# Optimization experiments

Hardware: AMD Instinct MI355X
Metric: run time of the kernel (lower is better)

## Reference

```python
import jax, jax.numpy as jnp
import numpy as np

N_NODES = 100000
N_EDGES = 1000000
NUM_GRAPHS = 500
EPS = 1e-5


def gcn_conv(x, src, dst, W, b, n_nodes):
    # PyG GCNConv: h = x @ W, symmetric norm with self-loops, aggregate at dst, add bias
    h = x @ W
    deg = jnp.zeros((n_nodes,), h.dtype).at[dst].add(1.0) + 1.0  # in-degree + self-loop
    dis = jax.lax.rsqrt(deg)
    msg = h[src] * (dis[src] * dis[dst])[:, None]               # [E, F] gather
    agg = jnp.zeros_like(h).at[dst].add(msg)                    # scatter-add
    return agg + h * (dis * dis)[:, None] + b                   # self-loop term + bias


def bn_eval(x, g, be, m, v):
    return (x - m) * jax.lax.rsqrt(v + EPS) * g + be


def setup_inputs() -> dict:
    key = jax.random.key(0)
    ks = jax.random.split(key, 8)
    edge_index = jax.random.randint(ks[0], (2, N_EDGES), 0, N_NODES, dtype=jnp.int32)
    batch = jnp.sort(jax.random.randint(ks[1], (N_NODES,), 0, NUM_GRAPHS, dtype=jnp.int32))
    d_in, h1, h2, hc, nc = 64, 64, 32, 16, 2
    return {
        "x": jax.random.normal(ks[2], (N_NODES, d_in), jnp.float32),
        "edge_index": edge_index,
        "batch": batch,
        "W1": jax.random.normal(ks[3], (d_in, h1), jnp.float32) / np.sqrt(d_in),
        "b1": jnp.zeros((h1,), jnp.float32),
        "g1": jnp.ones((h1,), jnp.float32),
        "be1": jnp.zeros((h1,), jnp.float32),
        "m1": jnp.zeros((h1,), jnp.float32),
        "v1": jnp.ones((h1,), jnp.float32),
        "W2": jax.random.normal(ks[4], (h1, h2), jnp.float32) / np.sqrt(h1),
        "b2": jnp.zeros((h2,), jnp.float32),
        "g2": jnp.ones((h2,), jnp.float32),
        "be2": jnp.zeros((h2,), jnp.float32),
        "m2": jnp.zeros((h2,), jnp.float32),
        "v2": jnp.ones((h2,), jnp.float32),
        "Wc1": jax.random.normal(ks[5], (h2, hc), jnp.float32) / np.sqrt(h2),
        "bc1": jnp.zeros((hc,), jnp.float32),
        "Wc2": jax.random.normal(ks[6], (hc, nc), jnp.float32) / np.sqrt(hc),
        "bc2": jnp.zeros((nc,), jnp.float32),
    }


def reference(x, edge_index, batch, W1, b1, g1, be1, m1, v1,
              W2, b2, g2, be2, m2, v2, Wc1, bc1, Wc2, bc2):
    src, dst = edge_index[0], edge_index[1]
    n = x.shape[0]
    # encoder layer 1: GCNConv -> BN(eval) -> ReLU  (dropout off in eval)
    h = jax.nn.relu(bn_eval(gcn_conv(x, src, dst, W1, b1, n), g1, be1, m1, v1))
    # encoder layer 2
    h = jax.nn.relu(bn_eval(gcn_conv(h, src, dst, W2, b2, n), g2, be2, m2, v2))
    # global mean pool over graphs
    sums = jax.ops.segment_sum(h, batch, num_segments=NUM_GRAPHS)
    cnts = jax.ops.segment_sum(jnp.ones((n,), h.dtype), batch, num_segments=NUM_GRAPHS)
    z = sums / jnp.maximum(cnts, 1.0)[:, None]                  # [NUM_GRAPHS, h2]
    # classifier MLP
    return jax.nn.relu(z @ Wc1 + bc1) @ Wc2 + bc2               # [NUM_GRAPHS, num_classes]
```

## Files before the change

kernel.cpp:

```cpp
#include <hip/hip_runtime.h>
#include <hip/hip_bf16.h>


#define CHUNK 4096
#define CAP   4096

typedef float floatx2 __attribute__((ext_vector_type(2)));

__global__ __launch_bounds__(256) void k_binpairs2(
    const int* __restrict__ src, const int* __restrict__ dst,
    int* __restrict__ bucketCursor, unsigned* __restrict__ pairs, int E) {
    __shared__ int lh[512];
    __shared__ int lbase[512];
    for (int i = threadIdx.x; i < 512; i += 256) lh[i] = 0;
    __syncthreads();
    int base = blockIdx.x * CHUNK;
    for (int i = threadIdx.x; i < CHUNK; i += 256) {
        int e = base + i;
        if (e < E) atomicAdd(&lh[dst[e] >> 8], 1);
    }
    __syncthreads();
    for (int i = threadIdx.x; i < 512; i += 256) {
        int c = lh[i];
        lbase[i] = c ? atomicAdd(&bucketCursor[i], c) : 0;
        lh[i] = 0;
    }
    __syncthreads();
    for (int i = threadIdx.x; i < CHUNK; i += 256) {
        int e = base + i;
        if (e < E) {
            int d = dst[e];
            int b = d >> 8;
            int r = atomicAdd(&lh[b], 1);
            pairs[(size_t)b * CAP + lbase[b] + r] =
                ((unsigned)src[e] << 8) | (unsigned)(d & 255);
        }
    }
}

__global__ __launch_bounds__(256) void k_csr2(
    const unsigned* __restrict__ pairs, const int* __restrict__ bucketCursor,
    int* __restrict__ rowStart, int* __restrict__ rowEnd,
    float* __restrict__ dis, int* __restrict__ perm, int n,
    float* __restrict__ sums, int nSums) {
    __shared__ int cnt[256];
    __shared__ int s[256];
    __shared__ int cur[256];
    int b = blockIdx.x, tid = threadIdx.x;
    int zi = b * 256 + tid;
    if (zi < nSums) sums[zi] = 0.f;
    int total = bucketCursor[b];
    size_t base = (size_t)b * CAP;
    cnt[tid] = 0;
    __syncthreads();
    for (int i = tid; i < total; i += 256) atomicAdd(&cnt[pairs[base + i] & 255], 1);
    __syncthreads();
    int v = cnt[tid];
    s[tid] = v;
    __syncthreads();
    for (int off = 1; off < 256; off <<= 1) {
        int t = (tid >= off) ? s[tid - off] : 0;
        __syncthreads();
        s[tid] += t;
        __syncthreads();
    }
    int excl = s[tid] - v;
    int node = b * 256 + tid;
    if (node < n) {
        rowStart[node] = (int)base + excl;
        rowEnd[node]   = (int)base + excl + v;
        dis[node] = rsqrtf((float)v + 1.0f);
    }
    cur[tid] = excl;
    __syncthreads();
    for (int i = tid; i < total; i += 256) {
        unsigned pr = pairs[base + i];
        int lo = pr & 255;
        int slot = atomicAdd(&cur[lo], 1);
        perm[base + slot] = (int)(pr >> 8);
    }
}

__global__ __launch_bounds__(256) void k_gemm64(
    const float* __restrict__ x, const float* __restrict__ W,
    const float* __restrict__ dis, unsigned char* __restrict__ hs8, int n) {
    __shared__ float Ws[64 * 64];
    __shared__ float xs[128][65];
    const int tid = threadIdx.x;
    for (int i = tid * 4; i < 4096; i += 1024)
        *(float4*)&Ws[i] = *(const float4*)&W[i];
    const int base = blockIdx.x * 128;
    for (int i = tid; i < 2048; i += 256) {
        int r = i >> 4;
        int k = (i & 15) * 4;
        int row = base + r;
        float4 xv = (row < n) ? *(const float4*)&x[(size_t)row * 64 + k]
                              : make_float4(0.f, 0.f, 0.f, 0.f);
        xs[r][k] = xv.x; xs[r][k + 1] = xv.y; xs[r][k + 2] = xv.z; xs[r][k + 3] = xv.w;
    }
    __syncthreads();
    const int cg = tid & 7;
    const int rg = tid >> 3;
    float acc[4][8] = {};
#pragma unroll 4
    for (int k = 0; k < 64; ++k) {
        float w8[8];
        *(float4*)&w8[0] = *(const float4*)&Ws[k * 64 + cg * 8];
        *(float4*)&w8[4] = *(const float4*)&Ws[k * 64 + cg * 8 + 4];
        float x4[4];
#pragma unroll
        for (int rr = 0; rr < 4; ++rr) x4[rr] = xs[rg * 4 + rr][k];
#pragma unroll
        for (int rr = 0; rr < 4; ++rr)
#pragma unroll
            for (int cc = 0; cc < 8; ++cc)
                acc[rr][cc] = fmaf(x4[rr], w8[cc], acc[rr][cc]);
    }
#pragma unroll
    for (int rr = 0; rr < 4; ++rr) {
        int row = base + rg * 4 + rr;
        if (row >= n) break;
        float d = dis[row];
        int q0 = __builtin_amdgcn_cvt_pk_fp8_f32(acc[rr][0] * d, acc[rr][1] * d, 0, false);
        q0 = __builtin_amdgcn_cvt_pk_fp8_f32(acc[rr][2] * d, acc[rr][3] * d, q0, true);
        int q1 = __builtin_amdgcn_cvt_pk_fp8_f32(acc[rr][4] * d, acc[rr][5] * d, 0, false);
        q1 = __builtin_amdgcn_cvt_pk_fp8_f32(acc[rr][6] * d, acc[rr][7] * d, q1, true);
        uint2 q = {(unsigned)q0, (unsigned)q1};
        *(uint2*)&hs8[(size_t)row * 64 + cg * 8] = q;
    }
}

__device__ __forceinline__ void unpack8(uint2 u, float* a) {
    floatx2 p0 = __builtin_amdgcn_cvt_pk_f32_fp8(u.x, false);
    floatx2 p1 = __builtin_amdgcn_cvt_pk_f32_fp8(u.x, true);
    floatx2 p2 = __builtin_amdgcn_cvt_pk_f32_fp8(u.y, false);
    floatx2 p3 = __builtin_amdgcn_cvt_pk_f32_fp8(u.y, true);
    a[0] = p0[0]; a[1] = p0[1]; a[2] = p1[0]; a[3] = p1[1];
    a[4] = p2[0]; a[5] = p2[1]; a[6] = p3[0]; a[7] = p3[1];
}

__global__ __launch_bounds__(256) void k_g64f8_gemm32(
    const unsigned char* __restrict__ hs8, const int* __restrict__ rowStart,
    const int* __restrict__ rowEnd, const int* __restrict__ perm,
    const float* __restrict__ dis,
    const float* __restrict__ b, const float* __restrict__ g,
    const float* __restrict__ be, const float* __restrict__ m,
    const float* __restrict__ v, const float* __restrict__ W2,
    unsigned char* __restrict__ hs2f8, int n) {
    __shared__ float W2s[64 * 32];
    __shared__ float actS[32][68];
    for (int i = threadIdx.x * 4; i < 2048; i += 1024)
        *(float4*)&W2s[i] = *(const float4*)&W2[i];
    __syncthreads();

    const uint2* hsu = (const uint2*)hs8;
    int c = threadIdx.x & 7;
    int ln = threadIdx.x >> 3;
    int node = (blockIdx.x * 256 + threadIdx.x) >> 3;
    if (node >= n) return;
    int r0 = rowStart[node], r1 = rowEnd[node];
    float d = dis[node];
    float a[8];
    unpack8(hsu[(size_t)node * 8 + c], a);
    int e = r0;
    for (; e + 7 < r1; e += 8) {
        int s0 = perm[e],     s1 = perm[e + 1], s2 = perm[e + 2], s3 = perm[e + 3];
        int s4 = perm[e + 4], s5 = perm[e + 5], s6 = perm[e + 6], s7 = perm[e + 7];
        uint2 u0 = hsu[(size_t)s0 * 8 + c];
        uint2 u1 = hsu[(size_t)s1 * 8 + c];
        uint2 u2 = hsu[(size_t)s2 * 8 + c];
        uint2 u3 = hsu[(size_t)s3 * 8 + c];
        uint2 u4 = hsu[(size_t)s4 * 8 + c];
        uint2 u5 = hsu[(size_t)s5 * 8 + c];
        uint2 u6 = hsu[(size_t)s6 * 8 + c];
        uint2 u7 = hsu[(size_t)s7 * 8 + c];
        float t[8];
#pragma unroll
        for (int j = 0; j < 8; ++j) {
            uint2 u = j == 0 ? u0 : j == 1 ? u1 : j == 2 ? u2 : j == 3 ? u3
                    : j == 4 ? u4 : j == 5 ? u5 : j == 6 ? u6 : u7;
            unpack8(u, t);
#pragma unroll
            for (int q = 0; q < 8; ++q) a[q] += t[q];
        }
    }
    for (; e < r1; ++e) {
        float t[8];
        unpack8(hsu[(size_t)perm[e] * 8 + c], t);
#pragma unroll
        for (int q = 0; q < 8; ++q) a[q] += t[q];
    }
    int f = 8 * c;
    float y[8];
#pragma unroll
    for (int h = 0; h < 2; ++h) {
        float4 gv = *(const float4*)&g[f + 4 * h];
        float4 vv = *(const float4*)&v[f + 4 * h];
        float4 bv = *(const float4*)&b[f + 4 * h];
        float4 mv = *(const float4*)&m[f + 4 * h];
        float4 bev = *(const float4*)&be[f + 4 * h];
        float sc0 = gv.x * rsqrtf(vv.x + 1e-5f), sc1 = gv.y * rsqrtf(vv.y + 1e-5f);
        float sc2 = gv.z * rsqrtf(vv.z + 1e-5f), sc3 = gv.w * rsqrtf(vv.w + 1e-5f);
        float y0 = fmaf(a[4 * h + 0] * d, sc0, (bv.x - mv.x) * sc0 + bev.x);
        float y1 = fmaf(a[4 * h + 1] * d, sc1, (bv.y - mv.y) * sc1 + bev.y);
        float y2 = fmaf(a[4 * h + 2] * d, sc2, (bv.z - mv.z) * sc2 + bev.z);
        float y3 = fmaf(a[4 * h + 3] * d, sc3, (bv.w - mv.w) * sc3 + bev.w);
        y[4 * h + 0] = y0 > 0.f ? y0 : 0.f;
        y[4 * h + 1] = y1 > 0.f ? y1 : 0.f;
        y[4 * h + 2] = y2 > 0.f ? y2 : 0.f;
        y[4 * h + 3] = y3 > 0.f ? y3 : 0.f;
    }
    *(float4*)&actS[ln][f]     = *(float4*)&y[0];
    *(float4*)&actS[ln][f + 4] = *(float4*)&y[4];

    float o0 = 0.f, o1 = 0.f, o2 = 0.f, o3 = 0.f;
#pragma unroll
    for (int k = 0; k < 64; ++k) {
        float av = actS[ln][k];
        float4 w = *(const float4*)&W2s[k * 32 + 4 * c];
        o0 = fmaf(av, w.x, o0);
        o1 = fmaf(av, w.y, o1);
        o2 = fmaf(av, w.z, o2);
        o3 = fmaf(av, w.w, o3);
    }
    int q = __builtin_amdgcn_cvt_pk_fp8_f32(o0 * d, o1 * d, 0, false);
    q = __builtin_amdgcn_cvt_pk_fp8_f32(o2 * d, o3 * d, q, true);
    *(unsigned*)&hs2f8[(size_t)node * 32 + 4 * c] = (unsigned)q;
}

__global__ __launch_bounds__(256) void k_g32f8_pool(
    const unsigned char* __restrict__ hs8, const int* __restrict__ rowStart,
    const int* __restrict__ rowEnd, const int* __restrict__ perm,
    const float* __restrict__ dis,
    const float* __restrict__ b, const float* __restrict__ g,
    const float* __restrict__ be, const float* __restrict__ m,
    const float* __restrict__ v, const int* __restrict__ batch,
    float* __restrict__ sums, float* __restrict__ cntG, int n) {
    __shared__ float lsum[64][32];
    __shared__ float lcnt[64];
    const uint2* hsu = (const uint2*)hs8;
    int tid = threadIdx.x;
    int c = tid & 3;
    int node = (blockIdx.x * 256 + tid) >> 2;
    int base = blockIdx.x * 64;
    bool valid = node < n;

    int lastNode = min(base + 63, n - 1);
    int g0 = batch[base < n ? base : n - 1];
    int span = batch[lastNode] - g0 + 1;
    bool ldsPath = span <= 64;

    if (ldsPath) {
        for (int i = tid; i < span * 32; i += 256) lsum[i >> 5][i & 31] = 0.f;
        for (int i = tid; i < span; i += 256) lcnt[i] = 0.f;
    }
    __syncthreads();

    float y[8];
    int f = 8 * c;
    if (valid) {
        int r0 = rowStart[node], r1 = rowEnd[node];
        float d = dis[node];
        float a[8];
        unpack8(hsu[(size_t)node * 4 + c], a);
        int e = r0;
        for (; e + 7 < r1; e += 8) {
            int s0 = perm[e],     s1 = perm[e + 1], s2 = perm[e + 2], s3 = perm[e + 3];
            int s4 = perm[e + 4], s5 = perm[e + 5], s6 = perm[e + 6], s7 = perm[e + 7];
            uint2 u0 = hsu[(size_t)s0 * 4 + c];
            uint2 u1 = hsu[(size_t)s1 * 4 + c];
            uint2 u2 = hsu[(size_t)s2 * 4 + c];
            uint2 u3 = hsu[(size_t)s3 * 4 + c];
            uint2 u4 = hsu[(size_t)s4 * 4 + c];
            uint2 u5 = hsu[(size_t)s5 * 4 + c];
            uint2 u6 = hsu[(size_t)s6 * 4 + c];
            uint2 u7 = hsu[(size_t)s7 * 4 + c];
            float t[8];
#pragma unroll
            for (int j = 0; j < 8; ++j) {
                uint2 u = j == 0 ? u0 : j == 1 ? u1 : j == 2 ? u2 : j == 3 ? u3
                        : j == 4 ? u4 : j == 5 ? u5 : j == 6 ? u6 : u7;
                unpack8(u, t);
#pragma unroll
                for (int q = 0; q < 8; ++q) a[q] += t[q];
            }
        }
        for (; e < r1; ++e) {
            float t[8];
            unpack8(hsu[(size_t)perm[e] * 4 + c], t);
#pragma unroll
            for (int q = 0; q < 8; ++q) a[q] += t[q];
        }
#pragma unroll
        for (int h = 0; h < 2; ++h) {
            float4 gv = *(const float4*)&g[f + 4 * h];
            float4 vv = *(const float4*)&v[f + 4 * h];
            float4 bv = *(const float4*)&b[f + 4 * h];
            float4 mv = *(const float4*)&m[f + 4 * h];
            float4 bev = *(const float4*)&be[f + 4 * h];
            float sc0 = gv.x * rsqrtf(vv.x + 1e-5f), sc1 = gv.y * rsqrtf(vv.y + 1e-5f);
            float sc2 = gv.z * rsqrtf(vv.z + 1e-5f), sc3 = gv.w * rsqrtf(vv.w + 1e-5f);
            float y0 = fmaf(a[4 * h + 0] * d, sc0, (bv.x - mv.x) * sc0 + bev.x);
            float y1 = fmaf(a[4 * h + 1] * d, sc1, (bv.y - mv.y) * sc1 + bev.y);
            float y2 = fmaf(a[4 * h + 2] * d, sc2, (bv.z - mv.z) * sc2 + bev.z);
            float y3 = fmaf(a[4 * h + 3] * d, sc3, (bv.w - mv.w) * sc3 + bev.w);
            y[4 * h + 0] = y0 > 0.f ? y0 : 0.f;
            y[4 * h + 1] = y1 > 0.f ? y1 : 0.f;
            y[4 * h + 2] = y2 > 0.f ? y2 : 0.f;
            y[4 * h + 3] = y3 > 0.f ? y3 : 0.f;
        }
        int bg = batch[node];
        if (ldsPath) {
            int gl = bg - g0;
#pragma unroll
            for (int j = 0; j < 8; ++j) atomicAdd(&lsum[gl][f + j], y[j]);
            if (c == 0) atomicAdd(&lcnt[gl], 1.f);
        } else {
#pragma unroll
            for (int j = 0; j < 8; ++j) atomicAdd(&sums[(size_t)bg * 32 + f + j], y[j]);
            if (c == 0) atomicAdd(&cntG[bg], 1.f);
        }
    }
    __syncthreads();
    if (ldsPath) {
        for (int i = tid; i < span * 32; i += 256) {
            int gs = i >> 5, ff = i & 31;
            float vl = lsum[gs][ff];
            if (vl != 0.f) atomicAdd(&sums[(size_t)(g0 + gs) * 32 + ff], vl);
        }
        for (int i = tid; i < span; i += 256) {
            float vl = lcnt[i];
            if (vl != 0.f) atomicAdd(&cntG[g0 + i], vl);
        }
    }
}

__global__ void k_mlp(const float* __restrict__ sums, const float* __restrict__ cnt,
                      const float* __restrict__ Wc1, const float* __restrict__ bc1,
                      const float* __restrict__ Wc2, const float* __restrict__ bc2,
                      float* __restrict__ out, int G) {
    int g = blockIdx.x * blockDim.x + threadIdx.x;
    if (g >= G) return;
    float c = cnt[g];
    c = c < 1.f ? 1.f : c;
    float inv = 1.f / c;
    float z[32];
#pragma unroll
    for (int j = 0; j < 32; ++j) z[j] = sums[(size_t)g * 32 + j] * inv;
    float o0 = bc2[0], o1 = bc2[1];
#pragma unroll
    for (int k = 0; k < 16; ++k) {
        float t = bc1[k];
#pragma unroll
        for (int j = 0; j < 32; ++j) t = fmaf(z[j], Wc1[j * 16 + k], t);
        t = t > 0.f ? t : 0.f;
        o0 = fmaf(t, Wc2[k * 2 + 0], o0);
        o1 = fmaf(t, Wc2[k * 2 + 1], o1);
    }
    out[g * 2 + 0] = o0;
    out[g * 2 + 1] = o1;
}

extern "C" void kernel_launch(void* const* d_in, const int* in_sizes, int n_in,
                              void* d_out, int out_size, void* d_ws, size_t ws_size,
                              hipStream_t stream) {
    const float* x   = (const float*)d_in[0];
    const int* ei    = (const int*)d_in[1];
    const int* batch = (const int*)d_in[2];
    const float* W1  = (const float*)d_in[3];
    const float* b1  = (const float*)d_in[4];
    const float* g1  = (const float*)d_in[5];
    const float* be1 = (const float*)d_in[6];
    const float* m1  = (const float*)d_in[7];
    const float* v1  = (const float*)d_in[8];
    const float* W2  = (const float*)d_in[9];
    const float* b2  = (const float*)d_in[10];
    const float* g2  = (const float*)d_in[11];
    const float* be2 = (const float*)d_in[12];
    const float* m2  = (const float*)d_in[13];
    const float* v2  = (const float*)d_in[14];
    const float* Wc1 = (const float*)d_in[15];
    const float* bc1 = (const float*)d_in[16];
    const float* Wc2 = (const float*)d_in[17];
    const float* bc2 = (const float*)d_in[18];

    const int n = in_sizes[2];
    const int E = in_sizes[1] / 2;
    const int G = out_size / 2;
    const int* srcI = ei;
    const int* dstI = ei + E;
    const int NB = (n + 255) >> 8;

    char* pw = (char*)d_ws;
    auto alloc = [&](size_t bytes) {
        char* r = pw;
        pw += (bytes + 255) & ~(size_t)255;
        return r;
    };
    float*    dis          = (float*)alloc((size_t)n * 4);
    int*      bucketCursor = (int*)alloc(512 * 4);
    unsigned* pairs        = (unsigned*)alloc((size_t)NB * CAP * 4);
    int*      perm         = (int*)alloc((size_t)NB * CAP * 4);
    int*      rowStart     = (int*)alloc((size_t)n * 4);
    int*      rowEnd       = (int*)alloc((size_t)n * 4);
    unsigned char* hs1f8   = (unsigned char*)alloc((size_t)64 * n);
    unsigned char* hs2f8   = (unsigned char*)alloc((size_t)32 * n);
    float*    sums         = (float*)alloc((size_t)32 * G * 4 + (size_t)G * 4);
    float*    cntG         = sums + (size_t)32 * G;

    const int NT = 256;
    const int nbE = (E + CHUNK - 1) / CHUNK;
    const int nSums = G * 33;

    hipMemsetAsync(bucketCursor, 0, 512 * 4, stream);
    k_binpairs2<<<nbE, NT, 0, stream>>>(srcI, dstI, bucketCursor, pairs, E);
    k_csr2<<<NB, NT, 0, stream>>>(pairs, bucketCursor, rowStart, rowEnd, dis, perm,
                                  n, sums, nSums);

    k_gemm64<<<(n + 127) / 128, NT, 0, stream>>>(x, W1, dis, hs1f8, n);
    k_g64f8_gemm32<<<(n * 8 + NT - 1) / NT, NT, 0, stream>>>(
        hs1f8, rowStart, rowEnd, perm, dis, b1, g1, be1, m1, v1, W2, hs2f8, n);

    k_g32f8_pool<<<(n * 4 + NT - 1) / NT, NT, 0, stream>>>(
        hs2f8, rowStart, rowEnd, perm, dis, b2, g2, be2, m2, v2, batch,
        sums, cntG, n);

    k_mlp<<<(G + NT - 1) / NT, NT, 0, stream>>>(sums, cntG, Wc1, bc1, Wc2, bc2,
                                                (float*)d_out, G);
}
```

Before: 130.1 us.

## Fuse edge binning with first GEMM and move source normalization into gather

```diff
diff --git a/kernel.cpp b/kernel.cpp
--- a/kernel.cpp
+++ b/kernel.cpp
@@ -7,34 +7,88 @@
 
 typedef float floatx2 __attribute__((ext_vector_type(2)));
 
-__global__ __launch_bounds__(256) void k_binpairs2(
+union SMemP {
+    struct { int lh[512]; int lbase[512]; } bp;
+    struct { float Ws[64 * 64]; float xs[128][65]; } gm;
+};
+
+__global__ __launch_bounds__(256) void k_prep(
     const int* __restrict__ src, const int* __restrict__ dst,
-    int* __restrict__ bucketCursor, unsigned* __restrict__ pairs, int E) {
-    __shared__ int lh[512];
-    __shared__ int lbase[512];
-    for (int i = threadIdx.x; i < 512; i += 256) lh[i] = 0;
-    __syncthreads();
-    int base = blockIdx.x * CHUNK;
-    for (int i = threadIdx.x; i < CHUNK; i += 256) {
-        int e = base + i;
-        if (e < E) atomicAdd(&lh[dst[e] >> 8], 1);
-    }
-    __syncthreads();
-    for (int i = threadIdx.x; i < 512; i += 256) {
-        int c = lh[i];
-        lbase[i] = c ? atomicAdd(&bucketCursor[i], c) : 0;
-        lh[i] = 0;
-    }
-    __syncthreads();
-    for (int i = threadIdx.x; i < CHUNK; i += 256) {
-        int e = base + i;
-        if (e < E) {
-            int d = dst[e];
-            int b = d >> 8;
-            int r = atomicAdd(&lh[b], 1);
-            pairs[(size_t)b * CAP + lbase[b] + r] =
-                ((unsigned)src[e] << 8) | (unsigned)(d & 255);
-        }
+    int* __restrict__ bucketCursor, unsigned* __restrict__ pairs, int E,
+    const float* __restrict__ x, const float* __restrict__ W,
+    unsigned char* __restrict__ hs8, int n, int nbE) {
+    __shared__ SMemP sm;
+    const int tid = threadIdx.x;
+
+    if ((int)blockIdx.x < nbE) {
+        for (int i = tid; i < 512; i += 256) sm.bp.lh[i] = 0;
+        __syncthreads();
+        int base = blockIdx.x * CHUNK;
+        for (int i = tid; i < CHUNK; i += 256) {
+            int e = base + i;
+            if (e < E) atomicAdd(&sm.bp.lh[dst[e] >> 8], 1);
+        }
+        __syncthreads();
+        for (int i = tid; i < 512; i += 256) {
+            int c = sm.bp.lh[i];
+            sm.bp.lbase[i] = c ? atomicAdd(&bucketCursor[i], c) : 0;
+            sm.bp.lh[i] = 0;
+        }
+        __syncthreads();
+        for (int i = tid; i < CHUNK; i += 256) {
+            int e = base + i;
+            if (e < E) {
+                int d = dst[e];
+                int b = d >> 8;
+                int r = atomicAdd(&sm.bp.lh[b], 1);
+                pairs[(size_t)b * CAP + sm.bp.lbase[b] + r] =
+                    ((unsigned)src[e] << 8) | (unsigned)(d & 255);
+            }
+        }
+        return;
+    }
+
+    const int tile = (int)blockIdx.x - nbE;
+    for (int i = tid * 4; i < 4096; i += 1024)
+        *(float4*)&sm.gm.Ws[i] = *(const float4*)&W[i];
+    const int base = tile * 128;
+    for (int i = tid; i < 2048; i += 256) {
+        int r = i >> 4;
+        int k = (i & 15) * 4;
+        int row = base + r;
+        float4 xv = (row < n) ? *(const float4*)&x[(size_t)row * 64 + k]
+                              : make_float4(0.f, 0.f, 0.f, 0.f);
+        sm.gm.xs[r][k] = xv.x; sm.gm.xs[r][k + 1] = xv.y;
+        sm.gm.xs[r][k + 2] = xv.z; sm.gm.xs[r][k + 3] = xv.w;
+    }
+    __syncthreads();
+    const int cg = tid & 7;
+    const int rg = tid >> 3;
+    float acc[4][8] = {};
+#pragma unroll 4
+    for (int k = 0; k < 64; ++k) {
+        float w8[8];
+        *(float4*)&w8[0] = *(const float4*)&sm.gm.Ws[k * 64 + cg * 8];
+        *(float4*)&w8[4] = *(const float4*)&sm.gm.Ws[k * 64 + cg * 8 + 4];
+        float x4[4];
+#pragma unroll
+        for (int rr = 0; rr < 4; ++rr) x4[rr] = sm.gm.xs[rg * 4 + rr][k];
+#pragma unroll
+        for (int rr = 0; rr < 4; ++rr)
+#pragma unroll
+            for (int cc = 0; cc < 8; ++cc)
+                acc[rr][cc] = fmaf(x4[rr], w8[cc], acc[rr][cc]);
+    }
+#pragma unroll
+    for (int rr = 0; rr < 4; ++rr) {
+        int row = base + rg * 4 + rr;
+        if (row >= n) break;
+        int q0 = __builtin_amdgcn_cvt_pk_fp8_f32(acc[rr][0], acc[rr][1], 0, false);
+        q0 = __builtin_amdgcn_cvt_pk_fp8_f32(acc[rr][2], acc[rr][3], q0, true);
+        int q1 = __builtin_amdgcn_cvt_pk_fp8_f32(acc[rr][4], acc[rr][5], 0, false);
+        q1 = __builtin_amdgcn_cvt_pk_fp8_f32(acc[rr][6], acc[rr][7], q1, true);
+        uint2 q = {(unsigned)q0, (unsigned)q1};
+        *(uint2*)&hs8[(size_t)row * 64 + cg * 8] = q;
     }
 }
 
@@ -81,55 +135,6 @@
     }
 }
 
-__global__ __launch_bounds__(256) void k_gemm64(
-    const float* __restrict__ x, const float* __restrict__ W,
-    const float* __restrict__ dis, unsigned char* __restrict__ hs8, int n) {
-    __shared__ float Ws[64 * 64];
-    __shared__ float xs[128][65];
-    const int tid = threadIdx.x;
-    for (int i = tid * 4; i < 4096; i += 1024)
-        *(float4*)&Ws[i] = *(const float4*)&W[i];
-    const int base = blockIdx.x * 128;
-    for (int i = tid; i < 2048; i += 256) {
-        int r = i >> 4;
-        int k = (i & 15) * 4;
-        int row = base + r;
-        float4 xv = (row < n) ? *(const float4*)&x[(size_t)row * 64 + k]
-                              : make_float4(0.f, 0.f, 0.f, 0.f);
-        xs[r][k] = xv.x; xs[r][k + 1] = xv.y; xs[r][k + 2] = xv.z; xs[r][k + 3] = xv.w;
-    }
-    __syncthreads();
-    const int cg = tid & 7;
-    const int rg = tid >> 3;
-    float acc[4][8] = {};
-#pragma unroll 4
-    for (int k = 0; k < 64; ++k) {
-        float w8[8];
-        *(float4*)&w8[0] = *(const float4*)&Ws[k * 64 + cg * 8];
-        *(float4*)&w8[4] = *(const float4*)&Ws[k * 64 + cg * 8 + 4];
-        float x4[4];
-#pragma unroll
-        for (int rr = 0; rr < 4; ++rr) x4[rr] = xs[rg * 4 + rr][k];
-#pragma unroll
-        for (int rr = 0; rr < 4; ++rr)
-#pragma unroll
-            for (int cc = 0; cc < 8; ++cc)
-                acc[rr][cc] = fmaf(x4[rr], w8[cc], acc[rr][cc]);
-    }
-#pragma unroll
-    for (int rr = 0; rr < 4; ++rr) {
-        int row = base + rg * 4 + rr;
-        if (row >= n) break;
-        float d = dis[row];
-        int q0 = __builtin_amdgcn_cvt_pk_fp8_f32(acc[rr][0] * d, acc[rr][1] * d, 0, false);
-        q0 = __builtin_amdgcn_cvt_pk_fp8_f32(acc[rr][2] * d, acc[rr][3] * d, q0, true);
-        int q1 = __builtin_amdgcn_cvt_pk_fp8_f32(acc[rr][4] * d, acc[rr][5] * d, 0, false);
-        q1 = __builtin_amdgcn_cvt_pk_fp8_f32(acc[rr][6] * d, acc[rr][7] * d, q1, true);
-        uint2 q = {(unsigned)q0, (unsigned)q1};
-        *(uint2*)&hs8[(size_t)row * 64 + cg * 8] = q;
-    }
-}
-
 __device__ __forceinline__ void unpack8(uint2 u, float* a) {
     floatx2 p0 = __builtin_amdgcn_cvt_pk_f32_fp8(u.x, false);
     floatx2 p1 = __builtin_amdgcn_cvt_pk_f32_fp8(u.x, true);
@@ -162,6 +167,8 @@
     float d = dis[node];
     float a[8];
     unpack8(hsu[(size_t)node * 8 + c], a);
+#pragma unroll
+    for (int q = 0; q < 8; ++q) a[q] *= d;
     int e = r0;
     for (; e + 7 < r1; e += 8) {
         int s0 = perm[e],     s1 = perm[e + 1], s2 = perm[e + 2], s3 = perm[e + 3];
@@ -174,21 +181,27 @@
         uint2 u5 = hsu[(size_t)s5 * 8 + c];
         uint2 u6 = hsu[(size_t)s6 * 8 + c];
         uint2 u7 = hsu[(size_t)s7 * 8 + c];
+        float d0 = dis[s0], d1 = dis[s1], d2 = dis[s2], d3 = dis[s3];
+        float d4 = dis[s4], d5 = dis[s5], d6 = dis[s6], d7 = dis[s7];
         float t[8];
 #pragma unroll
         for (int j = 0; j < 8; ++j) {
             uint2 u = j == 0 ? u0 : j == 1 ? u1 : j == 2 ? u2 : j == 3 ? u3
                     : j == 4 ? u4 : j == 5 ? u5 : j == 6 ? u6 : u7;
+            float ds = j == 0 ? d0 : j == 1 ? d1 : j == 2 ? d2 : j == 3 ? d3
+                     : j == 4 ? d4 : j == 5 ? d5 : j == 6 ? d6 : d7;
             unpack8(u, t);
 #pragma unroll
-            for (int q = 0; q < 8; ++q) a[q] += t[q];
+            for (int q = 0; q < 8; ++q) a[q] = fmaf(t[q], ds, a[q]);
         }
     }
     for (; e < r1; ++e) {
+        int s = perm[e];
+        float ds = dis[s];
         float t[8];
-        unpack8(hsu[(size_t)perm[e] * 8 + c], t);
-#pragma unroll
-        for (int q = 0; q < 8; ++q) a[q] += t[q];
+        unpack8(hsu[(size_t)s * 8 + c], t);
+#pragma unroll
+        for (int q = 0; q < 8; ++q) a[q] = fmaf(t[q], ds, a[q]);
     }
     int f = 8 * c;
     float y[8];
@@ -410,14 +423,15 @@
 
     const int NT = 256;
     const int nbE = (E + CHUNK - 1) / CHUNK;
+    const int ngemm = (n + 127) / 128;
     const int nSums = G * 33;
 
     hipMemsetAsync(bucketCursor, 0, 512 * 4, stream);
-    k_binpairs2<<<nbE, NT, 0, stream>>>(srcI, dstI, bucketCursor, pairs, E);
+    k_prep<<<nbE + ngemm, NT, 0, stream>>>(srcI, dstI, bucketCursor, pairs, E,
+                                           x, W1, hs1f8, n, nbE);
     k_csr2<<<NB, NT, 0, stream>>>(pairs, bucketCursor, rowStart, rowEnd, dis, perm,
                                   n, sums, nSums);
 
-    k_gemm64<<<(n + 127) / 128, NT, 0, stream>>>(x, W1, dis, hs1f8, n);
     k_g64f8_gemm32<<<(n * 8 + NT - 1) / NT, NT, 0, stream>>>(
         hs1f8, rowStart, rowEnd, perm, dis, b1, g1, be1, m1, v1, W2, hs2f8, n);
 
```

Result: faster. 122.1 us (-6.2%).
